# Optimization experiments

Measured on AMD Instinct MI355X. Metric: run time of the kernel, lower is better.

## Reference

```python
import jax, jax.numpy as jnp
import numpy as np

NUM_GRAPHS = 128
NUM_LAYERS = 3
D_IN = 64
D_H = 64
D_OUT = 10
N_NODES = 100000
N_EDGES = 1000000


def segment_softmax(scores, seg, num_segments):
    # numerically stable softmax over variable-size segments (per-destination-node)
    m = jax.ops.segment_max(scores, seg, num_segments=num_segments)
    ex = jnp.exp(scores - m[seg])
    s = jax.ops.segment_sum(ex, seg, num_segments=num_segments)
    return ex / (s[seg] + 1e-16)


def setup_inputs() -> dict:
    key = jax.random.key(0)
    ks = jax.random.split(key, 16)
    x = jax.random.normal(ks[0], (N_NODES, D_IN), dtype=jnp.float32)
    edge_index = jax.random.randint(ks[1], (2, N_EDGES), 0, N_NODES, dtype=jnp.int32)
    batch = jnp.sort(jax.random.randint(ks[2], (N_NODES,), 0, NUM_GRAPHS, dtype=jnp.int32))
    s = 0.05
    # stacked per-layer TransformerConv params (input_dim == hidden_dim so shapes align)
    Wq = jax.random.normal(ks[3], (NUM_LAYERS, D_H, D_H), dtype=jnp.float32) * s
    bq = jnp.zeros((NUM_LAYERS, D_H), dtype=jnp.float32)
    Wk = jax.random.normal(ks[4], (NUM_LAYERS, D_H, D_H), dtype=jnp.float32) * s
    bk = jnp.zeros((NUM_LAYERS, D_H), dtype=jnp.float32)
    Wv = jax.random.normal(ks[5], (NUM_LAYERS, D_H, D_H), dtype=jnp.float32) * s
    bv = jnp.zeros((NUM_LAYERS, D_H), dtype=jnp.float32)
    Ws = jax.random.normal(ks[6], (NUM_LAYERS, D_H, D_H), dtype=jnp.float32) * s  # root/skip lin
    bs = jnp.zeros((NUM_LAYERS, D_H), dtype=jnp.float32)
    W1 = jax.random.normal(ks[7], (D_H, D_H), dtype=jnp.float32) * s
    b1 = jnp.zeros((D_H,), dtype=jnp.float32)
    W2 = jax.random.normal(ks[8], (D_H, D_OUT), dtype=jnp.float32) * s
    b2 = jnp.zeros((D_OUT,), dtype=jnp.float32)
    return {"x": x, "edge_index": edge_index, "batch": batch,
            "Wq": Wq, "bq": bq, "Wk": Wk, "bk": bk, "Wv": Wv, "bv": bv,
            "Ws": Ws, "bs": bs, "W1": W1, "b1": b1, "W2": W2, "b2": b2}


def reference(x, edge_index, batch, Wq, bq, Wk, bk, Wv, bv, Ws, bs, W1, b1, W2, b2):
    n = x.shape[0]
    src, dst = edge_index[0], edge_index[1]  # PyG: edge_index[0]=source j, [1]=target i
    scale = 1.0 / jnp.sqrt(jnp.asarray(D_H, x.dtype))
    h = x
    pooled = []
    for l in range(NUM_LAYERS):
        q = h @ Wq[l] + bq[l]          # [N, d] query of target node
        k = h @ Wk[l] + bk[l]          # [N, d] key of source node
        v = h @ Wv[l] + bv[l]          # [N, d] value of source node
        scores = jnp.sum(q[dst] * k[src], axis=-1) * scale          # [E]
        alpha = segment_softmax(scores, dst, n)                     # softmax over in-edges
        agg = jax.ops.segment_sum(v[src] * alpha[:, None], dst, num_segments=n)  # [N, d]
        h = jax.nn.relu(agg + h @ Ws[l] + bs[l])                    # root_weight skip + relu
        pooled.append(jax.ops.segment_sum(h, batch, num_segments=NUM_GRAPHS))   # global_add_pool
    pooled_st = jnp.stack(pooled)                                   # [L, G, d]
    p = jax.nn.relu(pooled_st[-1] @ W1 + b1)                        # dropout p=0 / eval
    out = p @ W2 + b2                                               # [G, D_OUT]
    return out, pooled_st
```

## Files before the change

### kernel.cpp

```cpp
#include <hip/hip_runtime.h>
#include <hip/hip_bf16.h>
#include <math.h>

#define NN 100000
#define NE 1000000
#define DD 64
#define NG 128
#define NL 3

#define NBUK 196
#define EPB 2048
#define NBLK ((NE + EPB - 1) / EPB)
#define BCAP 6144
#define NDC 64

typedef unsigned short ushort_t;
typedef unsigned int u32;
typedef __attribute__((ext_vector_type(8))) short short8v;
typedef __attribute__((ext_vector_type(2))) float f32x2;
typedef __attribute__((ext_vector_type(4))) float f32x4;
typedef __attribute__((ext_vector_type(4))) unsigned int u32x4;

__device__ __forceinline__ ushort_t f2bf(float f) {
    __hip_bfloat16 h = __float2bfloat16(f);
    return *reinterpret_cast<ushort_t*>(&h);
}
__device__ __forceinline__ unsigned cvtpk(float lo, float hi) {
    unsigned r;
    asm("v_cvt_pk_bf16_f32 %0, %1, %2" : "=v"(r) : "v"(lo), "v"(hi));
    return r;
}
__device__ __forceinline__ f32x2 bfpair(u32 u) {
    f32x2 r;
    r.x = __builtin_bit_cast(float, u << 16);
    r.y = __builtin_bit_cast(float, u & 0xffff0000u);
    return r;
}
template <bool HI>
__device__ __forceinline__ f32x2 f8pair(u32 u) {
    return __builtin_amdgcn_cvt_pk_f32_fp8(u, HI);
}
__device__ __forceinline__ float sum8(float x) {
    int v = __builtin_bit_cast(int, x);
    x += __builtin_bit_cast(float, __builtin_amdgcn_update_dpp(0, v, 0xB1, 0xF, 0xF, true));
    v = __builtin_bit_cast(int, x);
    x += __builtin_bit_cast(float, __builtin_amdgcn_update_dpp(0, v, 0x4E, 0xF, 0xF, true));
    v = __builtin_bit_cast(int, x);
    x += __builtin_bit_cast(float, __builtin_amdgcn_update_dpp(0, v, 0x141, 0xF, 0xF, true));
    return x;
}


__global__ __launch_bounds__(256) void setup_k(const float* __restrict__ x, ushort_t* __restrict__ hbf,
                                               float* __restrict__ out, int totOut,
                                               int* __restrict__ gcur, int* __restrict__ gdh,
                                               const float* __restrict__ Wq, const float* __restrict__ Wk,
                                               const float* __restrict__ Wv, const float* __restrict__ Ws_,
                                               ushort_t* __restrict__ wpack,
                                               int cvtBlocks, int zeroBlocks) {
    int b = blockIdx.x, t = threadIdx.x;
    if (b < cvtBlocks) {
        int base = (b * 256 + t) * 4;
        float4 v = *(const float4*)&x[base];
        uint2 pk;
        pk.x = cvtpk(v.x, v.y);
        pk.y = cvtpk(v.z, v.w);
        *(uint2*)&hbf[base] = pk;
        return;
    }
    b -= cvtBlocks;
    if (b < zeroBlocks) {
        int i = b * 256 + t;
        if (i < totOut) out[i] = 0.f;
        if (b == 0 && t < NBUK) gcur[t] = 0;
        if (b == 1 && t < NDC) gdh[t] = 0;
        return;
    }
    b -= zeroBlocks;
    if (t < 64) {
        int mat = b & 3, layer = b >> 2;
        const float* W = ((mat == 0) ? Wq : (mat == 1) ? Wk : (mat == 2) ? Wv : Ws_) + layer * DD * DD;
        int lq = t >> 4, ln = t & 15;
#pragma unroll
        for (int ct = 0; ct < 4; ct++)
#pragma unroll
            for (int ks = 0; ks < 2; ks++)
#pragma unroll
                for (int j = 0; j < 8; j++) {
                    float v = W[(ks * 32 + lq * 8 + j) * DD + ct * 16 + ln];
                    wpack[((size_t)(b * 8 + ct * 2 + ks)) * 512 + t * 8 + j] = f2bf(v);
                }
    }
}


__global__ __launch_bounds__(256) void bin_k(const int* __restrict__ src,
                                             const int* __restrict__ dst,
                                             u32* __restrict__ binbuf,
                                             int* __restrict__ gcur) {
    __shared__ int hist[NBUK];
    __shared__ int excl[NBUK];
    __shared__ int cur[NBUK];
    __shared__ int gbase[NBUK];
    __shared__ int tmp[256];
    __shared__ u32 pairs[EPB];
    __shared__ unsigned char bukid[EPB];
    int t = threadIdx.x;
    int blk = blockIdx.x;
    int e0 = blk * EPB;
    int totvalid = NE - e0; if (totvalid > EPB) totvalid = EPB;

    for (int i = t; i < NBUK; i += 256) hist[i] = 0;
    __syncthreads();

    int mysrc[8], mydst[8];
#pragma unroll
    for (int i = 0; i < 8; i++) {
        int e = e0 + i * 256 + t;
        bool v = e < NE;
        mysrc[i] = v ? src[e] : -1;
        mydst[i] = v ? dst[e] : -1;
        if (v) atomicAdd(&hist[mydst[i] >> 9], 1);
    }
    __syncthreads();

    int v = (t < NBUK) ? hist[t] : 0;
    tmp[t] = v;
    __syncthreads();
#pragma unroll
    for (int off = 1; off < 256; off <<= 1) {
        int a = (t >= off) ? tmp[t - off] : 0;
        __syncthreads();
        tmp[t] += a;
        __syncthreads();
    }
    if (t < NBUK) { excl[t] = tmp[t] - v; cur[t] = tmp[t] - v; }
    __syncthreads();

#pragma unroll
    for (int i = 0; i < 8; i++) {
        if (mydst[i] >= 0) {
            int b = mydst[i] >> 9;
            int p = atomicAdd(&cur[b], 1);
            pairs[p] = ((u32)(mydst[i] & 511) << 17) | (u32)mysrc[i];
            bukid[p] = (unsigned char)b;
        }
    }
    if (t < NBUK && v > 0) gbase[t] = atomicAdd(&gcur[t], v);
    __syncthreads();

    for (int i = t; i < totvalid; i += 256) {
        int b = bukid[i];
        int idx = gbase[b] + (i - excl[b]);
        if (idx < BCAP) binbuf[(size_t)b * BCAP + idx] = pairs[i];
    }
}

__global__ __launch_bounds__(256) void csr_k(const u32* __restrict__ binbuf,
                                             const int* __restrict__ gcur,
                                             int* __restrict__ rowstart,
                                             int* __restrict__ csr_src) {
    __shared__ u32 pairs[BCAP];
    __shared__ int csrb[BCAP];
    __shared__ int deg[512];
    __shared__ int excl[512];
    __shared__ int cur[512];
    __shared__ int tmp[512];
    __shared__ int bt[256];
    int b = blockIdx.x;
    int t = threadIdx.x;

    int bv = 0;
    if (t < NBUK) { bv = gcur[t]; if (bv > BCAP) bv = BCAP; }
    bt[t] = bv;
    __syncthreads();
#pragma unroll
    for (int off = 1; off < 256; off <<= 1) {
        int a = (t >= off) ? bt[t - off] : 0;
        __syncthreads();
        bt[t] += a;
        __syncthreads();
    }
    int base = (b == 0) ? 0 : bt[b - 1];
    int T = bt[b] - base;
    if (b == 0 && t == 0) rowstart[NN] = bt[NBUK - 1];
    int nbase = b << 9;

    for (int i = t; i < 512; i += 256) deg[i] = 0;
    for (int i = t; i < T; i += 256) pairs[i] = binbuf[(size_t)b * BCAP + i];
    __syncthreads();
    for (int i = t; i < T; i += 256) atomicAdd(&deg[pairs[i] >> 17], 1);
    __syncthreads();

    int v0 = deg[t], v1 = deg[t + 256];
    tmp[t] = v0; tmp[t + 256] = v1;
    __syncthreads();
#pragma unroll
    for (int off = 1; off < 512; off <<= 1) {
        int a0 = (t >= off) ? tmp[t - off] : 0;
        int i1 = t + 256;
        int a1 = (i1 >= off) ? tmp[i1 - off] : 0;
        __syncthreads();
        tmp[t] += a0; tmp[i1] += a1;
        __syncthreads();
    }
    excl[t] = tmp[t] - v0; excl[t + 256] = tmp[t + 256] - v1;
    cur[t] = excl[t]; cur[t + 256] = excl[t + 256];
    __syncthreads();

    for (int i = t; i < 512; i += 256) {
        int n = nbase + i;
        if (n < NN) rowstart[n] = base + excl[i];
    }

    for (int i = t; i < T; i += 256) {
        u32 p = pairs[i];
        int pos = atomicAdd(&cur[p >> 17], 1);
        csrb[pos] = (int)(p & 0x1FFFFu);
    }
    __syncthreads();
    for (int i = t; i < T; i += 256) csr_src[base + i] = csrb[i];
}


__global__ __launch_bounds__(256) void dhist_k(const int* __restrict__ rowstart,
                                               int* __restrict__ gdh) {
    __shared__ int h[NDC];
    int t = threadIdx.x;
    if (t < NDC) h[t] = 0;
    __syncthreads();
    int n0 = blockIdx.x * 1024;
#pragma unroll
    for (int i = 0; i < 4; i++) {
        int n = n0 + i * 256 + t;
        if (n < NN) {
            int d = rowstart[n + 1] - rowstart[n];
            if (d > NDC - 1) d = NDC - 1;
            atomicAdd(&h[d], 1);
        }
    }
    __syncthreads();
    if (t < NDC && h[t]) atomicAdd(&gdh[t], h[t]);
}

__global__ __launch_bounds__(64) void dscan_k(const int* __restrict__ gdh,
                                              int* __restrict__ gdcur) {
    int t = threadIdx.x;
    int v = gdh[t];
    int inc = v;
#pragma unroll
    for (int off = 1; off < NDC; off <<= 1) {
        int u = __shfl_up(inc, off);
        if (t >= off) inc += u;
    }
    gdcur[t] = inc - v;
}

__global__ __launch_bounds__(256) void dperm_k(const int* __restrict__ rowstart,
                                               int* __restrict__ gdcur,
                                               int* __restrict__ perm) {
    __shared__ int h[NDC];
    __shared__ int cur[NDC];
    int t = threadIdx.x;
    if (t < NDC) h[t] = 0;
    __syncthreads();
    int n0 = blockIdx.x * 1024;
    int myd[4];
#pragma unroll
    for (int i = 0; i < 4; i++) {
        int n = n0 + i * 256 + t;
        myd[i] = -1;
        if (n < NN) {
            int d = rowstart[n + 1] - rowstart[n];
            if (d > NDC - 1) d = NDC - 1;
            myd[i] = d;
            atomicAdd(&h[d], 1);
        }
    }
    __syncthreads();
    if (t < NDC) cur[t] = h[t] ? atomicAdd(&gdcur[t], h[t]) : 0;
    __syncthreads();
#pragma unroll
    for (int i = 0; i < 4; i++) {
        if (myd[i] >= 0) {
            int pos = atomicAdd(&cur[myd[i]], 1);
            perm[pos] = n0 + i * 256 + t;
        }
    }
}


__global__ __launch_bounds__(256) void gemm4_k(const ushort_t* __restrict__ hbf,
                                               const ushort_t* __restrict__ wpl,
                                               const float* __restrict__ bq_, const float* __restrict__ bk_,
                                               const float* __restrict__ bv_, const float* __restrict__ bs_,
                                               ushort_t* __restrict__ qo, unsigned char* __restrict__ kv8,
                                               ushort_t* __restrict__ so) {
    int t = threadIdx.x;
    int lane = t & 63, wv = t >> 6;
    int ln = lane & 15, lq = lane >> 4;
    int rowbase = blockIdx.x * 64;

    const float* bsel = (wv == 0) ? bq_ : (wv == 1) ? bk_ : (wv == 2) ? bv_ : bs_;
    ushort_t* osel    = (wv == 0) ? qo : so;
    int kvoff = (wv == 1) ? 0 : 64;

    short8v wfrag[4][2];
#pragma unroll
    for (int ct = 0; ct < 4; ct++)
#pragma unroll
        for (int ks = 0; ks < 2; ks++)
            wfrag[ct][ks] = *(const short8v*)&wpl[((size_t)(wv * 8 + ct * 2 + ks)) * 512 + lane * 8];

    float4 bias[4];
#pragma unroll
    for (int ct = 0; ct < 4; ct++) bias[ct] = *(const float4*)&bsel[ct * 16 + lq * 4];

#pragma unroll
    for (int rt = 0; rt < 4; rt++) {
        int grow = rowbase + rt * 16 + ln;
        bool rv = grow < NN;
        int gr = rv ? grow : NN - 1;
        short8v h0 = *(const short8v*)&hbf[(size_t)gr * DD + lq * 8];
        short8v h1 = *(const short8v*)&hbf[(size_t)gr * DD + 32 + lq * 8];
#pragma unroll
        for (int ct = 0; ct < 4; ct++) {
            f32x4 acc;
            acc[0] = bias[ct].x; acc[1] = bias[ct].y; acc[2] = bias[ct].z; acc[3] = bias[ct].w;
            acc = __builtin_amdgcn_mfma_f32_16x16x32_bf16(wfrag[ct][0], h0, acc, 0, 0, 0);
            acc = __builtin_amdgcn_mfma_f32_16x16x32_bf16(wfrag[ct][1], h1, acc, 0, 0, 0);
            if (rv) {
                if (wv == 1 || wv == 2) {
                    int pk8 = __builtin_amdgcn_cvt_pk_fp8_f32(acc[0], acc[1], 0, false);
                    pk8 = __builtin_amdgcn_cvt_pk_fp8_f32(acc[2], acc[3], pk8, true);
                    *(u32*)&kv8[(size_t)grow * 128 + kvoff + ct * 16 + lq * 4] = (u32)pk8;
                } else {
                    uint2 pk;
                    pk.x = cvtpk(acc[0], acc[1]);
                    pk.y = cvtpk(acc[2], acc[3]);
                    *(uint2*)&osel[(size_t)grow * DD + ct * 16 + lq * 4] = pk;
                }
            }
        }
    }
}


#define SCLOG2E 0.18033688011112042f

__global__ __launch_bounds__(256) void agg_k(const ushort_t* __restrict__ qb,
                                             const unsigned char* __restrict__ kv8,
                                             const ushort_t* __restrict__ skb,
                                             const int* __restrict__ rowstart,
                                             const int* __restrict__ csr_src,
                                             const int* __restrict__ perm,
                                             ushort_t* __restrict__ hout) {
    int wv = threadIdx.x >> 6, lane = threadIdx.x & 63;
    int g = lane >> 3, j = lane & 7, sub = g & 1;
    int slot = blockIdx.x * 16 + wv * 4 + (g >> 1);
    if (slot >= NN) return;
    int nid = perm[slot];
    int r0 = rowstart[nid];
    int r1 = rowstart[nid + 1];

    u32x4 qa = *(const u32x4*)(qb + ((u32)nid << 6) + ((u32)j << 3));
    f32x2 q0 = bfpair(qa.x), q1 = bfpair(qa.y), q2 = bfpair(qa.z), q3 = bfpair(qa.w);

    float m = -1.0e38f, se = 0.f;
    f32x2 a0 = {0.f, 0.f}, a1 = {0.f, 0.f}, a2 = {0.f, 0.f}, a3 = {0.f, 0.f};

    int clampE = r1 - 1; if (clampE < 0) clampE = 0;
    int e0 = r0 + sub;
    int s0 = csr_src[e0 < clampE ? e0 : clampE];
    uint2 k0 = *(const uint2*)(kv8 + (size_t)s0 * 128 + 8 * j);
    uint2 v0 = *(const uint2*)(kv8 + (size_t)s0 * 128 + 64 + 8 * j);

    while (__ballot(e0 < r1)) {
        int e1 = e0 + 2;
        int s1 = csr_src[e1 < clampE ? e1 : clampE];
        uint2 k1 = *(const uint2*)(kv8 + (size_t)s1 * 128 + 8 * j);
        uint2 v1 = *(const uint2*)(kv8 + (size_t)s1 * 128 + 64 + 8 * j);

        f32x2 dp2 = q0 * f8pair<false>(k0.x);
        dp2 += q1 * f8pair<true >(k0.x);
        dp2 += q2 * f8pair<false>(k0.y);
        dp2 += q3 * f8pair<true >(k0.y);
        float dp = sum8(dp2.x + dp2.y);

        float w = 0.f;
        if (e0 < r1) {
            float sc = dp * SCLOG2E;
            if (sc <= m + 11.5f) { w = exp2f(sc - m); }
            else {
                float cc = exp2f(m - sc);
                se *= cc; a0 *= cc; a1 *= cc; a2 *= cc; a3 *= cc;
                m = sc; w = 1.f;
            }
        }
        se += w;
        a0 += f8pair<false>(v0.x) * w;
        a1 += f8pair<true >(v0.x) * w;
        a2 += f8pair<false>(v0.y) * w;
        a3 += f8pair<true >(v0.y) * w;

        e0 = e1; k0 = k1; v0 = v1;
    }

    float M = fmaxf(m, __shfl_xor(m, 8));
    float cc = exp2f(m - M);
    se *= cc; a0 *= cc; a1 *= cc; a2 *= cc; a3 *= cc;
    se += __shfl_xor(se, 8);
    a0.x += __shfl_xor(a0.x, 8); a0.y += __shfl_xor(a0.y, 8);
    a1.x += __shfl_xor(a1.x, 8); a1.y += __shfl_xor(a1.y, 8);
    a2.x += __shfl_xor(a2.x, 8); a2.y += __shfl_xor(a2.y, 8);
    a3.x += __shfl_xor(a3.x, 8); a3.y += __shfl_xor(a3.y, 8);

    if (sub == 0) {
        float inv = 1.0f / (se + 1e-16f);
        u32x4 sk = *(const u32x4*)(skb + ((u32)nid << 6) + ((u32)j << 3));
        f32x2 o0 = a0 * inv + bfpair(sk.x);
        f32x2 o1 = a1 * inv + bfpair(sk.y);
        f32x2 o2 = a2 * inv + bfpair(sk.z);
        f32x2 o3 = a3 * inv + bfpair(sk.w);
        u32x4 pk;
        pk.x = cvtpk(fmaxf(o0.x, 0.f), fmaxf(o0.y, 0.f));
        pk.y = cvtpk(fmaxf(o1.x, 0.f), fmaxf(o1.y, 0.f));
        pk.z = cvtpk(fmaxf(o2.x, 0.f), fmaxf(o2.y, 0.f));
        pk.w = cvtpk(fmaxf(o3.x, 0.f), fmaxf(o3.y, 0.f));
        *(u32x4*)(hout + ((u32)nid << 6) + ((u32)j << 3)) = pk;
    }
}


#define POOL_ROWS 128

__global__ __launch_bounds__(256) void pool_k(const ushort_t* __restrict__ h,
                                              const int* __restrict__ batch,
                                              float* __restrict__ pooled) {
    int i0 = blockIdx.x * POOL_ROWS;
    int i1 = i0 + POOL_ROWS; if (i1 > NN) i1 = NN;
    int lane = threadIdx.x & 63;
    int wv = threadIdx.x >> 6;
    float acc = 0.f;
    int gcur = -1;
    for (int i = i0 + wv; i < i1; i += 4) {
        int gi = batch[i];
        if (gi != gcur) {
            if (gcur >= 0) atomicAdd(&pooled[gcur * DD + lane], acc);
            gcur = gi; acc = 0.f;
        }
        unsigned u = ((unsigned)h[(size_t)i * DD + lane]) << 16;
        acc += __builtin_bit_cast(float, u);
    }
    if (gcur >= 0) atomicAdd(&pooled[gcur * DD + lane], acc);
}


__global__ __launch_bounds__(64) void head_k(const float* __restrict__ pooled2,
                                             const float* __restrict__ W1,
                                             const float* __restrict__ b1,
                                             const float* __restrict__ W2,
                                             const float* __restrict__ b2,
                                             float* __restrict__ out) {
    int g = blockIdx.x;
    int c = threadIdx.x;
    __shared__ float pg[64], p[64];
    pg[c] = pooled2[g * DD + c];
    __syncthreads();
    float a = b1[c];
#pragma unroll 8
    for (int kk = 0; kk < 64; kk++) a += pg[kk] * W1[kk * DD + c];
    p[c] = fmaxf(a, 0.f);
    __syncthreads();
    if (c < 10) {
        float o = b2[c];
#pragma unroll 8
        for (int kk = 0; kk < 64; kk++) o += p[kk] * W2[kk * 10 + c];
        out[g * 10 + c] = o;
    }
}


extern "C" void kernel_launch(void* const* d_in, const int* in_sizes, int n_in,
                              void* d_out, int out_size, void* d_ws, size_t ws_size,
                              hipStream_t stream) {
    const float* x    = (const float*)d_in[0];
    const int*   ei   = (const int*)d_in[1];
    const int*   batch= (const int*)d_in[2];
    const float* Wq   = (const float*)d_in[3];
    const float* bq   = (const float*)d_in[4];
    const float* Wk   = (const float*)d_in[5];
    const float* bk   = (const float*)d_in[6];
    const float* Wv   = (const float*)d_in[7];
    const float* bv   = (const float*)d_in[8];
    const float* Wsp  = (const float*)d_in[9];
    const float* bsp  = (const float*)d_in[10];
    const float* W1   = (const float*)d_in[11];
    const float* b1   = (const float*)d_in[12];
    const float* W2   = (const float*)d_in[13];
    const float* b2   = (const float*)d_in[14];
    float* out = (float*)d_out;
    float* pooled = out + NG * 10;

    const int* srcv = ei;
    const int* dstv = ei + NE;

    const size_t NEL = (size_t)NN * DD;
    ushort_t* hbf = (ushort_t*)d_ws;
    ushort_t* qb  = hbf + NEL;
    ushort_t* skb = qb  + NEL;
    unsigned char* kv8 = (unsigned char*)(skb + NEL);
    u32* binbuf   = (u32*)(kv8 + (size_t)NN * 128);
    int* gcur     = (int*)(binbuf + (size_t)NBUK * BCAP);
    int* gdh      = gcur + NBUK;
    int* gdcur    = gdh + NDC;
    int* rowstart = gdcur + NDC;
    int* csr_src  = rowstart + (NN + 1);
    int* perm     = csr_src + NE;
    ushort_t* wpack = (ushort_t*)(perm + NN);

    int totOut = NG * 10 + NL * NG * DD;
    int cvtBlocks = (int)(NEL / 4 / 256);
    int zeroBlocks = (totOut + 255) / 256;

    setup_k<<<cvtBlocks + zeroBlocks + NL * 4, 256, 0, stream>>>(
        x, hbf, out, totOut, gcur, gdh, Wq, Wk, Wv, Wsp, wpack, cvtBlocks, zeroBlocks);

    bin_k<<<NBLK, 256, 0, stream>>>(srcv, dstv, binbuf, gcur);
    csr_k<<<NBUK, 256, 0, stream>>>(binbuf, gcur, rowstart, csr_src);

    int dblocks = (NN + 1023) / 1024;
    dhist_k<<<dblocks, 256, 0, stream>>>(rowstart, gdh);
    dscan_k<<<1, 64, 0, stream>>>(gdh, gdcur);
    dperm_k<<<dblocks, 256, 0, stream>>>(rowstart, gdcur, perm);

    int gtiles = (NN + 63) / 64;
    int poolblocks = (NN + POOL_ROWS - 1) / POOL_ROWS;
    for (int l = 0; l < NL; l++) {
        gemm4_k<<<gtiles, 256, 0, stream>>>(hbf, wpack + (size_t)l * 4 * 8 * 512,
                                            bq + l * DD, bk + l * DD, bv + l * DD, bsp + l * DD,
                                            qb, kv8, skb);
        agg_k<<<(NN + 15) / 16, 256, 0, stream>>>(qb, kv8, skb, rowstart, csr_src, perm, hbf);
        pool_k<<<poolblocks, 256, 0, stream>>>(hbf, batch, pooled + l * NG * DD);
    }
    head_k<<<NG, 64, 0, stream>>>(pooled + 2 * NG * DD, W1, b1, W2, b2, out);
}
```

Measured before the change: 255.7 us.

## Fuse setup with edge binning, fold degree histogram into CSR, deepen agg prefetch

Splits zeroing into its own small kernel and merges the x/weight conversion blocks with the edge-binning blocks into one launch. The degree histogram now comes from the CSR build kernel, so the separate dhist pass is gone. The aggregation kernel walks the degree-sorted permutation in reverse, starting with the highest-degree nodes, and prefetches two edges ahead instead of one to hide gather latency. The cost is more live registers in agg_k and heavier shared-memory use in the fused kernel's conversion blocks.

```diff
diff --git a/kernel.cpp b/kernel.cpp
--- a/kernel.cpp
+++ b/kernel.cpp
@@ -51,13 +51,30 @@
 }
 
 
-__global__ __launch_bounds__(256) void setup_k(const float* __restrict__ x, ushort_t* __restrict__ hbf,
-                                               float* __restrict__ out, int totOut,
-                                               int* __restrict__ gcur, int* __restrict__ gdh,
+__global__ __launch_bounds__(256) void zero_k(float* __restrict__ out, int totOut,
+                                              int* __restrict__ gcur, int* __restrict__ gdh) {
+    int i = blockIdx.x * 256 + threadIdx.x;
+    if (i < totOut) out[i] = 0.f;
+    if (blockIdx.x == 0 && threadIdx.x < NBUK) gcur[threadIdx.x] = 0;
+    if (blockIdx.x == 1 && threadIdx.x < NDC) gdh[threadIdx.x] = 0;
+}
+
+
+__global__ __launch_bounds__(256) void fused_k(const float* __restrict__ x, ushort_t* __restrict__ hbf,
                                                const float* __restrict__ Wq, const float* __restrict__ Wk,
                                                const float* __restrict__ Wv, const float* __restrict__ Ws_,
                                                ushort_t* __restrict__ wpack,
-                                               int cvtBlocks, int zeroBlocks) {
+                                               const int* __restrict__ src, const int* __restrict__ dst,
+                                               u32* __restrict__ binbuf, int* __restrict__ gcur,
+                                               int cvtBlocks) {
+    __shared__ int hist[NBUK];
+    __shared__ int excl[NBUK];
+    __shared__ int cur[NBUK];
+    __shared__ int gbase[NBUK];
+    __shared__ int tmp[256];
+    __shared__ u32 pairs[EPB];
+    __shared__ unsigned char bukid[EPB];
+
     int b = blockIdx.x, t = threadIdx.x;
     if (b < cvtBlocks) {
         int base = (b * 256 + t) * 4;
@@ -69,45 +86,24 @@
         return;
     }
     b -= cvtBlocks;
-    if (b < zeroBlocks) {
-        int i = b * 256 + t;
-        if (i < totOut) out[i] = 0.f;
-        if (b == 0 && t < NBUK) gcur[t] = 0;
-        if (b == 1 && t < NDC) gdh[t] = 0;
+    if (b < NL * 4) {
+        if (t < 64) {
+            int mat = b & 3, layer = b >> 2;
+            const float* W = ((mat == 0) ? Wq : (mat == 1) ? Wk : (mat == 2) ? Wv : Ws_) + layer * DD * DD;
+#pragma unroll
+            for (int ct = 0; ct < 4; ct++)
+#pragma unroll
+                for (int ks = 0; ks < 2; ks++)
+#pragma unroll
+                    for (int j = 0; j < 8; j++) {
+                        float v = W[(ks * 32 + (t >> 4) * 8 + j) * DD + ct * 16 + (t & 15)];
+                        wpack[((size_t)(b * 8 + ct * 2 + ks)) * 512 + t * 8 + j] = f2bf(v);
+                    }
+        }
         return;
     }
-    b -= zeroBlocks;
-    if (t < 64) {
-        int mat = b & 3, layer = b >> 2;
-        const float* W = ((mat == 0) ? Wq : (mat == 1) ? Wk : (mat == 2) ? Wv : Ws_) + layer * DD * DD;
-        int lq = t >> 4, ln = t & 15;
-#pragma unroll
-        for (int ct = 0; ct < 4; ct++)
-#pragma unroll
-            for (int ks = 0; ks < 2; ks++)
-#pragma unroll
-                for (int j = 0; j < 8; j++) {
-                    float v = W[(ks * 32 + lq * 8 + j) * DD + ct * 16 + ln];
-                    wpack[((size_t)(b * 8 + ct * 2 + ks)) * 512 + t * 8 + j] = f2bf(v);
-                }
-    }
-}
-
-
-__global__ __launch_bounds__(256) void bin_k(const int* __restrict__ src,
-                                             const int* __restrict__ dst,
-                                             u32* __restrict__ binbuf,
-                                             int* __restrict__ gcur) {
-    __shared__ int hist[NBUK];
-    __shared__ int excl[NBUK];
-    __shared__ int cur[NBUK];
-    __shared__ int gbase[NBUK];
-    __shared__ int tmp[256];
-    __shared__ u32 pairs[EPB];
-    __shared__ unsigned char bukid[EPB];
-    int t = threadIdx.x;
-    int blk = blockIdx.x;
-    int e0 = blk * EPB;
+    b -= NL * 4;
+    int e0 = b * EPB;
     int totvalid = NE - e0; if (totvalid > EPB) totvalid = EPB;
 
     for (int i = t; i < NBUK; i += 256) hist[i] = 0;
@@ -140,26 +136,28 @@
 #pragma unroll
     for (int i = 0; i < 8; i++) {
         if (mydst[i] >= 0) {
-            int b = mydst[i] >> 9;
-            int p = atomicAdd(&cur[b], 1);
+            int bb = mydst[i] >> 9;
+            int p = atomicAdd(&cur[bb], 1);
             pairs[p] = ((u32)(mydst[i] & 511) << 17) | (u32)mysrc[i];
-            bukid[p] = (unsigned char)b;
+            bukid[p] = (unsigned char)bb;
         }
     }
     if (t < NBUK && v > 0) gbase[t] = atomicAdd(&gcur[t], v);
     __syncthreads();
 
     for (int i = t; i < totvalid; i += 256) {
-        int b = bukid[i];
-        int idx = gbase[b] + (i - excl[b]);
-        if (idx < BCAP) binbuf[(size_t)b * BCAP + idx] = pairs[i];
-    }
-}
+        int bb = bukid[i];
+        int idx = gbase[bb] + (i - excl[bb]);
+        if (idx < BCAP) binbuf[(size_t)bb * BCAP + idx] = pairs[i];
+    }
+}
+
 
 __global__ __launch_bounds__(256) void csr_k(const u32* __restrict__ binbuf,
                                              const int* __restrict__ gcur,
                                              int* __restrict__ rowstart,
-                                             int* __restrict__ csr_src) {
+                                             int* __restrict__ csr_src,
+                                             int* __restrict__ gdh) {
     __shared__ u32 pairs[BCAP];
     __shared__ int csrb[BCAP];
     __shared__ int deg[512];
@@ -167,6 +165,7 @@
     __shared__ int cur[512];
     __shared__ int tmp[512];
     __shared__ int bt[256];
+    __shared__ int ch[NDC];
     int b = blockIdx.x;
     int t = threadIdx.x;
 
@@ -187,10 +186,18 @@
     int nbase = b << 9;
 
     for (int i = t; i < 512; i += 256) deg[i] = 0;
+    if (t < NDC) ch[t] = 0;
     for (int i = t; i < T; i += 256) pairs[i] = binbuf[(size_t)b * BCAP + i];
     __syncthreads();
     for (int i = t; i < T; i += 256) atomicAdd(&deg[pairs[i] >> 17], 1);
     __syncthreads();
+
+    for (int i = t; i < 512; i += 256) {
+        if (nbase + i < NN) {
+            int d = deg[i]; if (d > NDC - 1) d = NDC - 1;
+            atomicAdd(&ch[d], 1);
+        }
+    }
 
     int v0 = deg[t], v1 = deg[t + 256];
     tmp[t] = v0; tmp[t + 256] = v1;
@@ -206,6 +213,7 @@
     }
     excl[t] = tmp[t] - v0; excl[t + 256] = tmp[t + 256] - v1;
     cur[t] = excl[t]; cur[t + 256] = excl[t + 256];
+    if (t < NDC && ch[t]) atomicAdd(&gdh[t], ch[t]);
     __syncthreads();
 
     for (int i = t; i < 512; i += 256) {
@@ -222,26 +230,6 @@
     for (int i = t; i < T; i += 256) csr_src[base + i] = csrb[i];
 }
 
-
-__global__ __launch_bounds__(256) void dhist_k(const int* __restrict__ rowstart,
-                                               int* __restrict__ gdh) {
-    __shared__ int h[NDC];
-    int t = threadIdx.x;
-    if (t < NDC) h[t] = 0;
-    __syncthreads();
-    int n0 = blockIdx.x * 1024;
-#pragma unroll
-    for (int i = 0; i < 4; i++) {
-        int n = n0 + i * 256 + t;
-        if (n < NN) {
-            int d = rowstart[n + 1] - rowstart[n];
-            if (d > NDC - 1) d = NDC - 1;
-            atomicAdd(&h[d], 1);
-        }
-    }
-    __syncthreads();
-    if (t < NDC && h[t]) atomicAdd(&gdh[t], h[t]);
-}
 
 __global__ __launch_bounds__(64) void dscan_k(const int* __restrict__ gdh,
                                               int* __restrict__ gdcur) {
@@ -359,7 +347,7 @@
     int g = lane >> 3, j = lane & 7, sub = g & 1;
     int slot = blockIdx.x * 16 + wv * 4 + (g >> 1);
     if (slot >= NN) return;
-    int nid = perm[slot];
+    int nid = perm[(NN - 1) - slot];
     int r0 = rowstart[nid];
     int r1 = rowstart[nid + 1];
 
@@ -370,16 +358,19 @@
     f32x2 a0 = {0.f, 0.f}, a1 = {0.f, 0.f}, a2 = {0.f, 0.f}, a3 = {0.f, 0.f};
 
     int clampE = r1 - 1; if (clampE < 0) clampE = 0;
-    int e0 = r0 + sub;
+    int e0 = r0 + sub, e1 = e0 + 2;
     int s0 = csr_src[e0 < clampE ? e0 : clampE];
+    int s1 = csr_src[e1 < clampE ? e1 : clampE];
     uint2 k0 = *(const uint2*)(kv8 + (size_t)s0 * 128 + 8 * j);
     uint2 v0 = *(const uint2*)(kv8 + (size_t)s0 * 128 + 64 + 8 * j);
+    uint2 k1 = *(const uint2*)(kv8 + (size_t)s1 * 128 + 8 * j);
+    uint2 v1 = *(const uint2*)(kv8 + (size_t)s1 * 128 + 64 + 8 * j);
 
     while (__ballot(e0 < r1)) {
-        int e1 = e0 + 2;
-        int s1 = csr_src[e1 < clampE ? e1 : clampE];
-        uint2 k1 = *(const uint2*)(kv8 + (size_t)s1 * 128 + 8 * j);
-        uint2 v1 = *(const uint2*)(kv8 + (size_t)s1 * 128 + 64 + 8 * j);
+        int e2 = e1 + 2;
+        int s2 = csr_src[e2 < clampE ? e2 : clampE];
+        uint2 k2 = *(const uint2*)(kv8 + (size_t)s2 * 128 + 8 * j);
+        uint2 v2 = *(const uint2*)(kv8 + (size_t)s2 * 128 + 64 + 8 * j);
 
         f32x2 dp2 = q0 * f8pair<false>(k0.x);
         dp2 += q1 * f8pair<true >(k0.x);
@@ -403,7 +394,8 @@
         a2 += f8pair<false>(v0.y) * w;
         a3 += f8pair<true >(v0.y) * w;
 
-        e0 = e1; k0 = k1; v0 = v1;
+        e0 = e1; e1 = e2;
+        k0 = k1; v0 = v1; k1 = k2; v1 = v2;
     }
 
     float M = fmaxf(m, __shfl_xor(m, 8));
@@ -523,16 +515,12 @@
     int cvtBlocks = (int)(NEL / 4 / 256);
     int zeroBlocks = (totOut + 255) / 256;
 
-    setup_k<<<cvtBlocks + zeroBlocks + NL * 4, 256, 0, stream>>>(
-        x, hbf, out, totOut, gcur, gdh, Wq, Wk, Wv, Wsp, wpack, cvtBlocks, zeroBlocks);
-
-    bin_k<<<NBLK, 256, 0, stream>>>(srcv, dstv, binbuf, gcur);
-    csr_k<<<NBUK, 256, 0, stream>>>(binbuf, gcur, rowstart, csr_src);
-
-    int dblocks = (NN + 1023) / 1024;
-    dhist_k<<<dblocks, 256, 0, stream>>>(rowstart, gdh);
+    zero_k<<<zeroBlocks, 256, 0, stream>>>(out, totOut, gcur, gdh);
+    fused_k<<<cvtBlocks + NL * 4 + NBLK, 256, 0, stream>>>(
+        x, hbf, Wq, Wk, Wv, Wsp, wpack, srcv, dstv, binbuf, gcur, cvtBlocks);
+    csr_k<<<NBUK, 256, 0, stream>>>(binbuf, gcur, rowstart, csr_src, gdh);
     dscan_k<<<1, 64, 0, stream>>>(gdh, gdcur);
-    dperm_k<<<dblocks, 256, 0, stream>>>(rowstart, gdcur, perm);
+    dperm_k<<<(NN + 1023) / 1024, 256, 0, stream>>>(rowstart, gdcur, perm);
 
     int gtiles = (NN + 63) / 64;
     int poolblocks = (NN + POOL_ROWS - 1) / POOL_ROWS;
```

New measurement: 253.0 us. About the same (-1.0%).
